# Performance work log

Measured on AMD Instinct MI355X. Metric: run time of the kernel, lower is better.

## Reference

```python
import jax, jax.numpy as jnp
import numpy as np
from math import factorial

LMAX = 5
MUL = 128            # multiplicity per irrep degree in the node embedding
NUM_CHANNELS = 4
NUM_RADII = 64
RES_BETA = 180
RES_ALPHA = 359
NUM_SPECIES = 5
NUM_GRAPHS = 16
NUM_NODES = 512
SH_DIM = (LMAX + 1) ** 2          # 36
EMB_DIM = MUL * SH_DIM            # 4608
NUM_IRREPS = MUL * (LMAX + 1)     # 768
INV_TEMP = 1.0


def _real_sh_basis(lmax, res_beta, res_alpha):
    """Orthonormal real spherical harmonics evaluated on a Gauss-Legendre beta grid
    and a uniform alpha grid (the grid used by e3nn.to_s2grid with gausslegendre
    quadrature). Returns B[(l*l + l + m), beta, alpha]. Precomputed in numpy since
    the grid is static."""
    y, _ = np.polynomial.legendre.leggauss(res_beta)          # y = cos(beta)
    alpha = np.linspace(0.0, 2.0 * np.pi, res_alpha, endpoint=False)
    # associated Legendre P[l, m] on y (Condon-Shortley phase)
    P = np.zeros((lmax + 1, lmax + 1, res_beta))
    P[0, 0] = 1.0
    somx2 = np.sqrt(np.clip(1.0 - y * y, 0.0, None))
    for m in range(1, lmax + 1):
        P[m, m] = -(2 * m - 1) * somx2 * P[m - 1, m - 1]
    for m in range(lmax):
        P[m + 1, m] = (2 * m + 1) * y * P[m, m]
    for m in range(lmax + 1):
        for l in range(m + 2, lmax + 1):
            P[l, m] = ((2 * l - 1) * y * P[l - 1, m] - (l + m - 1) * P[l - 2, m]) / (l - m)
    B = np.zeros(((lmax + 1) ** 2, res_beta, res_alpha))
    ones_a = np.ones_like(alpha)
    for l in range(lmax + 1):
        for m in range(l + 1):
            N = np.sqrt((2 * l + 1) / (4.0 * np.pi) * factorial(l - m) / factorial(l + m))
            if m == 0:
                B[l * l + l] = (N * P[l, 0])[:, None] * ones_a[None, :]
            else:
                B[l * l + l + m] = np.sqrt(2.0) * N * P[l, m][:, None] * np.cos(m * alpha)[None, :]
                B[l * l + l - m] = np.sqrt(2.0) * N * P[l, m][:, None] * np.sin(m * alpha)[None, :]
    return jnp.asarray(B, dtype=jnp.float32)


_B = _real_sh_basis(LMAX, RES_BETA, RES_ALPHA)   # (36, 180, 359)


def _split_blocks(emb):
    """Split an irreps array (G, sum_l MUL*(2l+1)) into per-degree blocks (G, MUL, 2l+1)."""
    blocks, off = [], 0
    for l in range(LMAX + 1):
        d = 2 * l + 1
        blocks.append(emb[:, off:off + MUL * d].reshape(-1, MUL, d))
        off += MUL * d
    return blocks


def setup_inputs() -> dict:
    key = jax.random.key(0)
    ks = jax.random.split(key, 13)
    inp = {
        "node_embeddings": jax.random.normal(ks[0], (NUM_NODES, EMB_DIM), jnp.float32),
        "species_embed": jax.random.normal(ks[1], (NUM_SPECIES, NUM_IRREPS), jnp.float32),
        "W_radial": jax.random.normal(ks[2], (MUL, NUM_RADII), jnp.float32),
        "W_mlp1": jax.random.normal(ks[3], (NUM_RADII, MUL), jnp.float32),
        "W_mlp2": jax.random.normal(ks[4], (MUL, NUM_RADII), jnp.float32),
    }
    for l in range(LMAX + 1):
        inp[f"W_ang_{l}"] = jax.random.normal(ks[5 + l], (MUL, NUM_CHANNELS), jnp.float32)
    inp["focus_indices"] = jax.random.randint(ks[11], (NUM_GRAPHS,), 0, NUM_NODES)
    inp["target_species"] = jax.random.randint(ks[12], (NUM_GRAPHS,), 0, NUM_SPECIES)
    return inp


def _forward(node_embeddings, species_embed, W_radial, W_mlp1, W_mlp2, W_ang,
             focus_indices, target_species):
    rsqrt_mul = np.float32(1.0 / np.sqrt(MUL))
    focus = node_embeddings[focus_indices]                 # (G, EMB_DIM)
    spec = species_embed[target_species]                   # (G, NUM_IRREPS), one scalar per irrep
    blocks = _split_blocks(focus)
    # target_species_embeddings * focus_node_embeddings: scale each irrep by its scalar
    scaled = [blk * spec[:, MUL * l:MUL * (l + 1), None] for l, blk in enumerate(blocks)]
    # radial path: e3nn Linear to num_radii x 0e (only 0e inputs contribute) + MLP
    scal0 = scaled[0][..., 0]                              # (G, MUL)
    r = (scal0 @ W_radial) * rsqrt_mul                     # (G, NUM_RADII)
    h = jax.nn.softplus((r @ W_mlp1) * np.float32(1.0 / np.sqrt(NUM_RADII)))
    radial_logits = (h @ W_mlp2) * rsqrt_mul               # (G, NUM_RADII)
    # angular path: e3nn Linear to num_channels * s2_irreps (per-degree channel mixing)
    ang = jnp.concatenate(
        [jnp.einsum("gkm,kc->gcm", scaled[l], W_ang[l]) * rsqrt_mul
         for l in range(LMAX + 1)], axis=-1)               # (G, C, 36)
    # joint distribution coefficients: radial logit adds to the l=0 coefficient
    joint0 = ang[:, :, None, :1] + radial_logits[:, None, :, None]     # (G, C, R, 1)
    rest = jnp.broadcast_to(ang[:, :, None, 1:],
                            (NUM_GRAPHS, NUM_CHANNELS, NUM_RADII, SH_DIM - 1))
    log_position_coeffs = jnp.concatenate([joint0, rest], axis=-1) * np.float32(INV_TEMP)
    # log_coeffs_to_logits: SH synthesis on the grid, then logsumexp over channels
    pos_grid = jnp.einsum("gcrk,kba->gcrba", log_position_coeffs, _B)
    position_logits = jax.nn.logsumexp(pos_grid, axis=1)   # (G, R, beta, alpha)
    ang_grid = jnp.einsum("gck,kba->gcba", ang, _B)
    angular_logits = jax.nn.logsumexp(ang_grid, axis=1, keepdims=True)  # (G, 1, beta, alpha)
    return log_position_coeffs, position_logits, angular_logits, radial_logits


def reference(node_embeddings, species_embed, W_radial, W_mlp1, W_mlp2,
              W_ang_0, W_ang_1, W_ang_2, W_ang_3, W_ang_4, W_ang_5,
              focus_indices, target_species):
    W_ang = [W_ang_0, W_ang_1, W_ang_2, W_ang_3, W_ang_4, W_ang_5]
    return _forward(node_embeddings, species_embed, W_radial, W_mlp1, W_mlp2, W_ang,
                    focus_indices, target_species)
```

## Files before the change

### kernel.cpp

```cpp
#include <hip/hip_runtime.h>
#include <math.h>

#define LMAX   5
#define MUL    128
#define NCH    4
#define NRAD   64
#define RBETA  180
#define RALPHA 359
#define NGRAPH 16
#define SH_DIM 36
#define EMB_DIM 4608
#define NIRR   768

#define GRID_BA (RBETA * RALPHA)
#define NW21    21
#define BTILE   4
#define NBT     (RBETA / BTILE)

typedef float vfloat4 __attribute__((ext_vector_type(4)));

#define OUT0_OFF 0
#define OUT1_OFF 147456
#define OUT2_OFF (147456 + 66170880)
#define OUT3_OFF (147456 + 66170880 + 1033920)

#define WS_TAB_OFF 0
#define WS_ANG_OFF 15360
#define WS_RAD_OFF 24576

__global__ __launch_bounds__(256)
void k_small(const float* __restrict__ ne, const float* __restrict__ sp,
             const float* __restrict__ wrad, const float* __restrict__ wm1,
             const float* __restrict__ wm2,
             const float* __restrict__ wa0, const float* __restrict__ wa1,
             const float* __restrict__ wa2, const float* __restrict__ wa3,
             const float* __restrict__ wa4, const float* __restrict__ wa5,
             const int* __restrict__ focus, const int* __restrict__ tspec,
             float* __restrict__ out0, float* __restrict__ out3,
             float* __restrict__ ang_ws, float* __restrict__ rad_ws,
             float* __restrict__ tab)
{
    const int tid = threadIdx.x;

    if (blockIdx.x == NGRAPH) {
        __shared__ double rcp[RBETA];
        for (int k = tid; k < RBETA; k += 256) rcp[k] = 1.0 / (double)(k + 1);
        __syncthreads();
        const int i = tid;
        if (i >= RBETA) return;
        const double PI = 3.14159265358979323846;
        double x = -cos(PI * (i + 0.75) / (RBETA + 0.5));
        for (int it = 0; it < 4; ++it) {
            double p0 = 1.0, p1 = x;
            for (int k = 1; k < RBETA; ++k) {
                double p2 = ((2.0 * k + 1.0) * x * p1 - (double)k * p0) * rcp[k];
                p0 = p1; p1 = p2;
            }
            double dp = RBETA * (x * p1 - p0) / (x * x - 1.0);
            x -= p1 / dp;
        }
        double P[LMAX + 1][LMAX + 1];
        P[0][0] = 1.0;
        double somx2 = sqrt(fmax(1.0 - x * x, 0.0));
        for (int m = 1; m <= LMAX; ++m) P[m][m] = -(2.0 * m - 1.0) * somx2 * P[m - 1][m - 1];
        for (int m = 0; m < LMAX; ++m)  P[m + 1][m] = (2.0 * m + 1.0) * x * P[m][m];
        for (int m = 0; m <= LMAX; ++m)
            for (int l = m + 2; l <= LMAX; ++l)
                P[l][m] = ((2.0 * l - 1.0) * x * P[l - 1][m] - (l + m - 1.0) * P[l - 2][m]) / (double)(l - m);
        const double FOURPI = 12.566370614359172;
        for (int l = 0; l <= LMAX; ++l) {
            for (int m = 0; m <= l; ++m) {
                double fr = 1.0;
                for (int k = l - m + 1; k <= l + m; ++k) fr /= (double)k;
                double N = sqrt((2.0 * l + 1.0) / FOURPI * fr);
                double w = N * P[l][m];
                if (m > 0) w *= 1.4142135623730951;
                tab[i * NW21 + l * (l + 1) / 2 + m] = (float)w;
            }
        }
        return;
    }

    __shared__ float s0[MUL];
    __shared__ float rr[NRAD];
    __shared__ float hh[MUL];
    __shared__ float rl[NRAD];
    __shared__ float sang[NCH * SH_DIM];

    const int g = blockIdx.x;
    const int fi = focus[g];
    const int ts = tspec[g];
    const float rs128 = 0.08838834764831845f;
    const float rs64  = 0.125f;

    if (tid < MUL) s0[tid] = ne[(size_t)fi * EMB_DIM + tid] * sp[ts * NIRR + tid];
    __syncthreads();

    if (tid < NRAD) {
        float acc = 0.f;
        for (int k = 0; k < MUL; ++k) acc += s0[k] * wrad[k * NRAD + tid];
        rr[tid] = acc * rs128;
    }
    __syncthreads();

    if (tid < MUL) {
        float acc = 0.f;
        for (int j = 0; j < NRAD; ++j) acc += rr[j] * wm1[j * MUL + tid];
        float x = acc * rs64;
        hh[tid] = fmaxf(x, 0.f) + log1pf(expf(-fabsf(x)));
    }
    __syncthreads();

    if (tid < NRAD) {
        float acc = 0.f;
        for (int k = 0; k < MUL; ++k) acc += hh[k] * wm2[k * NRAD + tid];
        float v = acc * rs128;
        rl[tid] = v;
        out3[g * NRAD + tid] = v;
        rad_ws[g * NRAD + tid] = v;
    }

    const float* WA[6] = {wa0, wa1, wa2, wa3, wa4, wa5};
    for (int t = tid; t < NCH * SH_DIM; t += blockDim.x) {
        int c = t / SH_DIM, kk = t % SH_DIM;
        int l = 0;
        while ((l + 1) * (l + 1) <= kk) ++l;
        int j = kk - l * l;
        int d = 2 * l + 1;
        const float* w  = WA[l];
        const float* nb = ne + (size_t)fi * EMB_DIM + MUL * l * l + j;
        const float* sb = sp + ts * NIRR + MUL * l;
        float acc = 0.f;
        for (int k = 0; k < MUL; ++k) acc += nb[k * d] * sb[k] * w[k * NCH + c];
        float v = acc * rs128;
        sang[t] = v;
        ang_ws[g * (NCH * SH_DIM) + t] = v;
    }
    __syncthreads();

    for (int t = tid; t < NCH * NRAD * SH_DIM; t += blockDim.x) {
        int kk = t % SH_DIM;
        int r  = (t / SH_DIM) % NRAD;
        int c  = t / (SH_DIM * NRAD);
        float v = sang[c * SH_DIM + kk];
        if (kk == 0) v += rl[r];
        out0[(size_t)g * (NCH * NRAD * SH_DIM) + t] = v;
    }
}

__global__ __launch_bounds__(256)
void k_fused(const float* __restrict__ tab, const float* __restrict__ ang_ws,
             const float* __restrict__ rad_ws,
             float* __restrict__ out1, float* __restrict__ out2)
{
    __shared__ float sW[BTILE][NW21];
    __shared__ float sAng[NCH * SH_DIM];
    __shared__ float sF[BTILE][NCH][11];
    __shared__ float sRC[NRAD];
    __shared__ __align__(16) float sL[BTILE * RALPHA];

    const int bt  = blockIdx.x;
    const int g   = blockIdx.y;
    const int tid = threadIdx.x;

    if (tid < BTILE * NW21)
        sW[tid / NW21][tid % NW21] = tab[(bt * BTILE + tid / NW21) * NW21 + tid % NW21];
    if (tid >= 128 && tid < 128 + NRAD)
        sRC[tid - 128] = rad_ws[g * NRAD + (tid - 128)] * 0.28209479177387814f;
    for (int t = tid; t < NCH * SH_DIM; t += 256)
        sAng[t] = ang_ws[g * (NCH * SH_DIM) + t];
    __syncthreads();

    if (tid < BTILE * NCH * 11) {
        int b = tid / (NCH * 11);
        int rem = tid % (NCH * 11);
        int c = rem / 11, j = rem % 11;
        const float* W = sW[b];
        float acc = 0.f;
        if (j == 0) {
            for (int l = 0; l <= LMAX; ++l)
                acc += sAng[c * SH_DIM + l * l + l] * W[l * (l + 1) / 2];
        } else if (j <= 5) {
            int m = j;
            for (int l = m; l <= LMAX; ++l)
                acc += sAng[c * SH_DIM + l * l + l + m] * W[l * (l + 1) / 2 + m];
        } else {
            int m = j - 5;
            for (int l = m; l <= LMAX; ++l)
                acc += sAng[c * SH_DIM + l * l + l - m] * W[l * (l + 1) / 2 + m];
        }
        sF[b][c][j] = acc;
    }
    __syncthreads();

    const float dalpha = 6.283185307179586f / 359.0f;
    for (int t = tid; t < BTILE * RALPHA; t += 256) {
        int b = t / RALPHA;
        int a = t % RALPHA;
        float alpha = dalpha * (float)a;
        float s1, c1;
        __sincosf(alpha, &s1, &c1);
        float t0 = sF[b][0][0], t1 = sF[b][1][0], t2 = sF[b][2][0], t3 = sF[b][3][0];
        float cm = c1, sm = s1;
        for (int m = 1; m <= 5; ++m) {
            t0 += sF[b][0][m] * cm + sF[b][0][5 + m] * sm;
            t1 += sF[b][1][m] * cm + sF[b][1][5 + m] * sm;
            t2 += sF[b][2][m] * cm + sF[b][2][5 + m] * sm;
            t3 += sF[b][3][m] * cm + sF[b][3][5 + m] * sm;
            float cn = cm * c1 - sm * s1;
            float sn = sm * c1 + cm * s1;
            cm = cn; sm = sn;
        }
        float mx = fmaxf(fmaxf(t0, t1), fmaxf(t2, t3));
        float s = expf(t0 - mx) + expf(t1 - mx) + expf(t2 - mx) + expf(t3 - mx);
        sL[t] = mx + logf(s);
    }
    __syncthreads();

    const vfloat4* srcL = (const vfloat4*)sL;
    const int N4 = (BTILE * RALPHA) / 4;

    {
        vfloat4* dst2 = (vfloat4*)(out2 + (size_t)g * GRID_BA + bt * (BTILE * RALPHA));
        for (int t = tid; t < N4; t += 256)
            dst2[t] = srcL[t];
    }
    float* base1 = out1 + (size_t)g * NRAD * GRID_BA + bt * (BTILE * RALPHA);
    for (int r = 0; r < NRAD; ++r) {
        const float rc = sRC[r];
        vfloat4* dst = (vfloat4*)(base1 + (size_t)r * GRID_BA);
        for (int t = tid; t < N4; t += 256)
            dst[t] = srcL[t] + rc;
    }
}

extern "C" void kernel_launch(void* const* d_in, const int* in_sizes, int n_in,
                              void* d_out, int out_size, void* d_ws, size_t ws_size,
                              hipStream_t stream) {
    const float* ne   = (const float*)d_in[0];
    const float* sp   = (const float*)d_in[1];
    const float* wrad = (const float*)d_in[2];
    const float* wm1  = (const float*)d_in[3];
    const float* wm2  = (const float*)d_in[4];
    const float* wa0  = (const float*)d_in[5];
    const float* wa1  = (const float*)d_in[6];
    const float* wa2  = (const float*)d_in[7];
    const float* wa3  = (const float*)d_in[8];
    const float* wa4  = (const float*)d_in[9];
    const float* wa5  = (const float*)d_in[10];
    const int* focus  = (const int*)d_in[11];
    const int* tspec  = (const int*)d_in[12];

    float* out  = (float*)d_out;
    float* out0 = out + OUT0_OFF;
    float* out1 = out + OUT1_OFF;
    float* out2 = out + OUT2_OFF;
    float* out3 = out + OUT3_OFF;

    float* tab    = (float*)((char*)d_ws + WS_TAB_OFF);
    float* ang_ws = (float*)((char*)d_ws + WS_ANG_OFF);
    float* rad_ws = (float*)((char*)d_ws + WS_RAD_OFF);

    hipLaunchKernelGGL(k_small, dim3(NGRAPH + 1), dim3(256), 0, stream,
                       ne, sp, wrad, wm1, wm2, wa0, wa1, wa2, wa3, wa4, wa5,
                       focus, tspec, out0, out3, ang_ws, rad_ws, tab);
    hipLaunchKernelGGL(k_fused, dim3(NBT, NGRAPH), dim3(256), 0, stream,
                       tab, ang_ws, rad_ws, out1, out2);
}
```

Measured before the change: 341.8 us.

## Fuse per-graph MLP and angular projection into grid synthesis kernel

The per-graph radial MLP and angular weight projection move from a separate small kernel into every block of the main grid-synthesis kernel. Each block recomputes them and keeps the results in shared memory, and only the bt==0 block writes out0 and out3. The Gauss-Legendre table is still built by its own single-block kernel. This drops the workspace round trip for angular and radial values and the serial dependency on a 17-block kernel, at the cost of redundant small GEMV work in all 45 beta-tile blocks per graph.

```diff
diff --git a/kernel.cpp b/kernel.cpp
--- a/kernel.cpp
+++ b/kernel.cpp
@@ -25,75 +25,82 @@
 #define OUT3_OFF (147456 + 66170880 + 1033920)
 
 #define WS_TAB_OFF 0
-#define WS_ANG_OFF 15360
-#define WS_RAD_OFF 24576
 
 __global__ __launch_bounds__(256)
-void k_small(const float* __restrict__ ne, const float* __restrict__ sp,
-             const float* __restrict__ wrad, const float* __restrict__ wm1,
-             const float* __restrict__ wm2,
-             const float* __restrict__ wa0, const float* __restrict__ wa1,
-             const float* __restrict__ wa2, const float* __restrict__ wa3,
-             const float* __restrict__ wa4, const float* __restrict__ wa5,
-             const int* __restrict__ focus, const int* __restrict__ tspec,
-             float* __restrict__ out0, float* __restrict__ out3,
-             float* __restrict__ ang_ws, float* __restrict__ rad_ws,
-             float* __restrict__ tab)
+void k_tab(float* __restrict__ tab)
 {
     const int tid = threadIdx.x;
-
-    if (blockIdx.x == NGRAPH) {
-        __shared__ double rcp[RBETA];
-        for (int k = tid; k < RBETA; k += 256) rcp[k] = 1.0 / (double)(k + 1);
-        __syncthreads();
-        const int i = tid;
-        if (i >= RBETA) return;
-        const double PI = 3.14159265358979323846;
-        double x = -cos(PI * (i + 0.75) / (RBETA + 0.5));
-        for (int it = 0; it < 4; ++it) {
-            double p0 = 1.0, p1 = x;
-            for (int k = 1; k < RBETA; ++k) {
-                double p2 = ((2.0 * k + 1.0) * x * p1 - (double)k * p0) * rcp[k];
-                p0 = p1; p1 = p2;
-            }
-            double dp = RBETA * (x * p1 - p0) / (x * x - 1.0);
-            x -= p1 / dp;
-        }
-        double P[LMAX + 1][LMAX + 1];
-        P[0][0] = 1.0;
-        double somx2 = sqrt(fmax(1.0 - x * x, 0.0));
-        for (int m = 1; m <= LMAX; ++m) P[m][m] = -(2.0 * m - 1.0) * somx2 * P[m - 1][m - 1];
-        for (int m = 0; m < LMAX; ++m)  P[m + 1][m] = (2.0 * m + 1.0) * x * P[m][m];
-        for (int m = 0; m <= LMAX; ++m)
-            for (int l = m + 2; l <= LMAX; ++l)
-                P[l][m] = ((2.0 * l - 1.0) * x * P[l - 1][m] - (l + m - 1.0) * P[l - 2][m]) / (double)(l - m);
-        const double FOURPI = 12.566370614359172;
-        for (int l = 0; l <= LMAX; ++l) {
-            for (int m = 0; m <= l; ++m) {
-                double fr = 1.0;
-                for (int k = l - m + 1; k <= l + m; ++k) fr /= (double)k;
-                double N = sqrt((2.0 * l + 1.0) / FOURPI * fr);
-                double w = N * P[l][m];
-                if (m > 0) w *= 1.4142135623730951;
-                tab[i * NW21 + l * (l + 1) / 2 + m] = (float)w;
-            }
-        }
-        return;
-    }
-
+    __shared__ double rcp[RBETA];
+    for (int k = tid; k < RBETA; k += 256) rcp[k] = 1.0 / (double)(k + 1);
+    __syncthreads();
+    const int i = tid;
+    if (i >= RBETA) return;
+    const double PI = 3.14159265358979323846;
+    double x = -cos(PI * (i + 0.75) / (RBETA + 0.5));
+    for (int it = 0; it < 4; ++it) {
+        double p0 = 1.0, p1 = x;
+        for (int k = 1; k < RBETA; ++k) {
+            double p2 = ((2.0 * k + 1.0) * x * p1 - (double)k * p0) * rcp[k];
+            p0 = p1; p1 = p2;
+        }
+        double dp = RBETA * (x * p1 - p0) / (x * x - 1.0);
+        x -= p1 / dp;
+    }
+    double P[LMAX + 1][LMAX + 1];
+    P[0][0] = 1.0;
+    double somx2 = sqrt(fmax(1.0 - x * x, 0.0));
+    for (int m = 1; m <= LMAX; ++m) P[m][m] = -(2.0 * m - 1.0) * somx2 * P[m - 1][m - 1];
+    for (int m = 0; m < LMAX; ++m)  P[m + 1][m] = (2.0 * m + 1.0) * x * P[m][m];
+    for (int m = 0; m <= LMAX; ++m)
+        for (int l = m + 2; l <= LMAX; ++l)
+            P[l][m] = ((2.0 * l - 1.0) * x * P[l - 1][m] - (l + m - 1.0) * P[l - 2][m]) / (double)(l - m);
+    const double FOURPI = 12.566370614359172;
+    for (int l = 0; l <= LMAX; ++l) {
+        for (int m = 0; m <= l; ++m) {
+            double fr = 1.0;
+            for (int k = l - m + 1; k <= l + m; ++k) fr /= (double)k;
+            double N = sqrt((2.0 * l + 1.0) / FOURPI * fr);
+            double w = N * P[l][m];
+            if (m > 0) w *= 1.4142135623730951;
+            tab[i * NW21 + l * (l + 1) / 2 + m] = (float)w;
+        }
+    }
+}
+
+__global__ __launch_bounds__(256)
+void k_all(const float* __restrict__ tab,
+           const float* __restrict__ ne, const float* __restrict__ sp,
+           const float* __restrict__ wrad, const float* __restrict__ wm1,
+           const float* __restrict__ wm2,
+           const float* __restrict__ wa0, const float* __restrict__ wa1,
+           const float* __restrict__ wa2, const float* __restrict__ wa3,
+           const float* __restrict__ wa4, const float* __restrict__ wa5,
+           const int* __restrict__ focus, const int* __restrict__ tspec,
+           float* __restrict__ out0, float* __restrict__ out1,
+           float* __restrict__ out2, float* __restrict__ out3)
+{
     __shared__ float s0[MUL];
     __shared__ float rr[NRAD];
     __shared__ float hh[MUL];
     __shared__ float rl[NRAD];
     __shared__ float sang[NCH * SH_DIM];
-
-    const int g = blockIdx.x;
-    const int fi = focus[g];
-    const int ts = tspec[g];
+    __shared__ float sW[BTILE][NW21];
+    __shared__ float sF[BTILE][NCH][11];
+    __shared__ float sRC[NRAD];
+    __shared__ __align__(16) float sL[BTILE * RALPHA];
+
+    const int bt  = blockIdx.x;
+    const int g   = blockIdx.y;
+    const int tid = threadIdx.x;
+    const int fi  = focus[g];
+    const int ts  = tspec[g];
     const float rs128 = 0.08838834764831845f;
     const float rs64  = 0.125f;
 
-    if (tid < MUL) s0[tid] = ne[(size_t)fi * EMB_DIM + tid] * sp[ts * NIRR + tid];
+    if (tid < BTILE * NW21)
+        sW[tid / NW21][tid % NW21] = tab[(bt * BTILE + tid / NW21) * NW21 + tid % NW21];
+    if (tid >= 128 && tid < 128 + MUL)
+        s0[tid - 128] = ne[(size_t)fi * EMB_DIM + (tid - 128)] * sp[ts * NIRR + (tid - 128)];
     __syncthreads();
 
     if (tid < NRAD) {
@@ -115,13 +122,13 @@
         float acc = 0.f;
         for (int k = 0; k < MUL; ++k) acc += hh[k] * wm2[k * NRAD + tid];
         float v = acc * rs128;
-        rl[tid] = v;
-        out3[g * NRAD + tid] = v;
-        rad_ws[g * NRAD + tid] = v;
+        rl[tid]  = v;
+        sRC[tid] = v * 0.28209479177387814f;
+        if (bt == 0) out3[g * NRAD + tid] = v;
     }
 
     const float* WA[6] = {wa0, wa1, wa2, wa3, wa4, wa5};
-    for (int t = tid; t < NCH * SH_DIM; t += blockDim.x) {
+    for (int t = tid; t < NCH * SH_DIM; t += 256) {
         int c = t / SH_DIM, kk = t % SH_DIM;
         int l = 0;
         while ((l + 1) * (l + 1) <= kk) ++l;
@@ -132,43 +139,8 @@
         const float* sb = sp + ts * NIRR + MUL * l;
         float acc = 0.f;
         for (int k = 0; k < MUL; ++k) acc += nb[k * d] * sb[k] * w[k * NCH + c];
-        float v = acc * rs128;
-        sang[t] = v;
-        ang_ws[g * (NCH * SH_DIM) + t] = v;
-    }
-    __syncthreads();
-
-    for (int t = tid; t < NCH * NRAD * SH_DIM; t += blockDim.x) {
-        int kk = t % SH_DIM;
-        int r  = (t / SH_DIM) % NRAD;
-        int c  = t / (SH_DIM * NRAD);
-        float v = sang[c * SH_DIM + kk];
-        if (kk == 0) v += rl[r];
-        out0[(size_t)g * (NCH * NRAD * SH_DIM) + t] = v;
-    }
-}
-
-__global__ __launch_bounds__(256)
-void k_fused(const float* __restrict__ tab, const float* __restrict__ ang_ws,
-             const float* __restrict__ rad_ws,
-             float* __restrict__ out1, float* __restrict__ out2)
-{
-    __shared__ float sW[BTILE][NW21];
-    __shared__ float sAng[NCH * SH_DIM];
-    __shared__ float sF[BTILE][NCH][11];
-    __shared__ float sRC[NRAD];
-    __shared__ __align__(16) float sL[BTILE * RALPHA];
-
-    const int bt  = blockIdx.x;
-    const int g   = blockIdx.y;
-    const int tid = threadIdx.x;
-
-    if (tid < BTILE * NW21)
-        sW[tid / NW21][tid % NW21] = tab[(bt * BTILE + tid / NW21) * NW21 + tid % NW21];
-    if (tid >= 128 && tid < 128 + NRAD)
-        sRC[tid - 128] = rad_ws[g * NRAD + (tid - 128)] * 0.28209479177387814f;
-    for (int t = tid; t < NCH * SH_DIM; t += 256)
-        sAng[t] = ang_ws[g * (NCH * SH_DIM) + t];
+        sang[t] = acc * rs128;
+    }
     __syncthreads();
 
     if (tid < BTILE * NCH * 11) {
@@ -179,17 +151,28 @@
         float acc = 0.f;
         if (j == 0) {
             for (int l = 0; l <= LMAX; ++l)
-                acc += sAng[c * SH_DIM + l * l + l] * W[l * (l + 1) / 2];
+                acc += sang[c * SH_DIM + l * l + l] * W[l * (l + 1) / 2];
         } else if (j <= 5) {
             int m = j;
             for (int l = m; l <= LMAX; ++l)
-                acc += sAng[c * SH_DIM + l * l + l + m] * W[l * (l + 1) / 2 + m];
+                acc += sang[c * SH_DIM + l * l + l + m] * W[l * (l + 1) / 2 + m];
         } else {
             int m = j - 5;
             for (int l = m; l <= LMAX; ++l)
-                acc += sAng[c * SH_DIM + l * l + l - m] * W[l * (l + 1) / 2 + m];
+                acc += sang[c * SH_DIM + l * l + l - m] * W[l * (l + 1) / 2 + m];
         }
         sF[b][c][j] = acc;
+    }
+
+    if (bt == 0) {
+        for (int t = tid; t < NCH * NRAD * SH_DIM; t += 256) {
+            int kk = t % SH_DIM;
+            int r  = (t / SH_DIM) % NRAD;
+            int c  = t / (SH_DIM * NRAD);
+            float v = sang[c * SH_DIM + kk];
+            if (kk == 0) v += rl[r];
+            out0[(size_t)g * (NCH * NRAD * SH_DIM) + t] = v;
+        }
     }
     __syncthreads();
 
@@ -257,13 +240,10 @@
     float* out2 = out + OUT2_OFF;
     float* out3 = out + OUT3_OFF;
 
-    float* tab    = (float*)((char*)d_ws + WS_TAB_OFF);
-    float* ang_ws = (float*)((char*)d_ws + WS_ANG_OFF);
-    float* rad_ws = (float*)((char*)d_ws + WS_RAD_OFF);
-
-    hipLaunchKernelGGL(k_small, dim3(NGRAPH + 1), dim3(256), 0, stream,
-                       ne, sp, wrad, wm1, wm2, wa0, wa1, wa2, wa3, wa4, wa5,
-                       focus, tspec, out0, out3, ang_ws, rad_ws, tab);
-    hipLaunchKernelGGL(k_fused, dim3(NBT, NGRAPH), dim3(256), 0, stream,
-                       tab, ang_ws, rad_ws, out1, out2);
+    float* tab = (float*)((char*)d_ws + WS_TAB_OFF);
+
+    hipLaunchKernelGGL(k_tab, dim3(1), dim3(256), 0, stream, tab);
+    hipLaunchKernelGGL(k_all, dim3(NBT, NGRAPH), dim3(256), 0, stream,
+                       tab, ne, sp, wrad, wm1, wm2, wa0, wa1, wa2, wa3, wa4, wa5,
+                       focus, tspec, out0, out1, out2, out3);
 }
```

Measured after the change: 356.9 us. +4.4%, slower.
